# Kernel optimization log

Measured on AMD Instinct MI355X. Metric: run time of the kernel, lower is better.

## Reference

```python
import jax, jax.numpy as jnp
import numpy as np
import math

N_HEADS = 16
ROPE_BASE = 10000.0


def _rope_interleaved(t, cos, sin):
    # t: [B,H,T,dk]; cos/sin: [T, dk//2] broadcast over B,H
    te, to = t[..., 0::2], t[..., 1::2]
    re = te * cos - to * sin
    ro = te * sin + to * cos
    # interleave back: [..., dk//2, 2] -> [..., dk]
    return jnp.stack([re, ro], axis=-1).reshape(t.shape)


def setup_inputs() -> dict:
    key = jax.random.key(0)
    ks = jax.random.split(key, 5)
    B, T, C = 2, 2048, 1024
    s = 1.0 / math.sqrt(C)
    return {
        "x": jax.random.normal(ks[0], (B, T, C), dtype=jnp.float32),
        "W_qkv": jax.random.normal(ks[1], (C, 3 * C), dtype=jnp.float32) * s,
        "b_qkv": jax.random.normal(ks[2], (3 * C,), dtype=jnp.float32) * 0.02,
        "W_proj": jax.random.normal(ks[3], (C, C), dtype=jnp.float32) * s,
        "b_proj": jax.random.normal(ks[4], (C,), dtype=jnp.float32) * 0.02,
    }


def reference(x, W_qkv, b_qkv, W_proj, b_proj):
    B, T, C = x.shape
    H = N_HEADS
    dk = C // H

    qkv = x @ W_qkv + b_qkv                      # [B,T,3C]
    q, k, v = jnp.split(qkv, 3, axis=-1)
    q = q.reshape(B, T, H, dk).transpose(0, 2, 1, 3)  # [B,H,T,dk]
    k = k.reshape(B, T, H, dk).transpose(0, 2, 1, 3)
    v = v.reshape(B, T, H, dk).transpose(0, 2, 1, 3)

    # RoPE angles: pos * base^(-2i/dk)
    freqs = ROPE_BASE ** (-2.0 * jnp.arange(dk // 2, dtype=jnp.float32) / dk)
    angles = jnp.arange(T, dtype=jnp.float32)[:, None] * freqs[None, :]  # [T,dk//2]
    cos, sin = jnp.cos(angles), jnp.sin(angles)

    q = _rope_interleaved(q, cos, sin)
    k = _rope_interleaved(k, cos, sin)

    attn = jnp.einsum("bhqd,bhkd->bhqk", q, k) / math.sqrt(dk)  # [B,H,T,T]
    causal = jnp.triu(jnp.full((T, T), -jnp.inf, dtype=attn.dtype), k=1)
    attn = jax.nn.softmax(attn + causal, axis=-1)

    scores = jnp.einsum("bhqk,bhkd->bhqd", attn, v)  # [B,H,T,dk]
    scores = scores.transpose(0, 2, 1, 3).reshape(B, T, C)
    return scores @ W_proj + b_proj
```

## Files before the change

kernel.cpp:

```cpp
#include <hip/hip_runtime.h>
#include <hip/hip_bf16.h>

typedef __bf16 bf16x8 __attribute__((ext_vector_type(8)));
typedef float f32x4 __attribute__((ext_vector_type(4)));
typedef float f32x16 __attribute__((ext_vector_type(16)));
typedef unsigned short u16;
typedef u16 u16x8 __attribute__((ext_vector_type(8)));

__device__ __forceinline__ u16 f2bf(float f) {
  union { float f; unsigned u; } v; v.f = f;
  unsigned r = v.u + 0x7fffu + ((v.u >> 16) & 1u);
  return (u16)(r >> 16);
}
__device__ __forceinline__ float bf2f(u16 u) {
  union { unsigned u; float f; } v; v.u = (unsigned)u << 16; return v.f;
}
__device__ __forceinline__ unsigned cvtpk(float a, float b) {
  unsigned r;
  asm("v_cvt_pk_bf16_f32 %0, %1, %2" : "=v"(r) : "v"(a), "v"(b));
  return r;
}
__device__ __forceinline__ float exp2_(float x) {
  float r;
  asm("v_exp_f32 %0, %1" : "=v"(r) : "v"(x));
  return r;
}
__device__ __forceinline__ float sin2pi_(float x) {
  float r;
  asm("v_sin_f32 %0, %1" : "=v"(r) : "v"(x));
  return r;
}
__device__ __forceinline__ float cos2pi_(float x) {
  float r;
  asm("v_cos_f32 %0, %1" : "=v"(r) : "v"(x));
  return r;
}
__device__ __forceinline__ void gload16(const void* g, void* l) {
  __builtin_amdgcn_global_load_lds(
      (__attribute__((address_space(1))) void*)(void*)g,
      (__attribute__((address_space(3))) void*)l, 16, 0, 0);
}

union U8 { bf16x8 v; unsigned u[4]; };

__global__ __launch_bounds__(256) void cast_x_k(const float* __restrict__ x,
                                                u16* __restrict__ xb, int n8) {
  int id = blockIdx.x * 256 + threadIdx.x;
  if (id >= n8) return;
  const float4* p = (const float4*)(x + (size_t)id * 8);
  float4 a = p[0], b = p[1];
  u16x8 o;
  o[0] = f2bf(a.x); o[1] = f2bf(a.y); o[2] = f2bf(a.z); o[3] = f2bf(a.w);
  o[4] = f2bf(b.x); o[5] = f2bf(b.y); o[6] = f2bf(b.z); o[7] = f2bf(b.w);
  *(u16x8*)(xb + (size_t)id * 8) = o;
}

__global__ __launch_bounds__(256) void tcast_k(const float* __restrict__ W,
                                               u16* __restrict__ Wt, int R, int Cc) {
  __shared__ float tile[32][33];
  int bx = blockIdx.x * 32, by = blockIdx.y * 32;
  int tx = threadIdx.x & 31, ty = threadIdx.x >> 5;
#pragma unroll
  for (int j = 0; j < 4; j++)
    tile[ty + j * 8][tx] = W[(size_t)(by + ty + j * 8) * Cc + bx + tx];
  __syncthreads();
#pragma unroll
  for (int j = 0; j < 4; j++)
    Wt[(size_t)(bx + ty + j * 8) * R + by + tx] = f2bf(tile[tx][ty + j * 8]);
}

template <bool BF16OUT>
__global__ __launch_bounds__(256) void gemm_bt_k(const u16* __restrict__ A,
                                                 const u16* __restrict__ Bt,
                                                 const float* __restrict__ bias,
                                                 void* __restrict__ Cv,
                                                 int M, int N, int K) {
  __shared__ u16 As[128 * 64];
  __shared__ u16 Bs[128 * 64];
  int tid = threadIdx.x;
  int m0 = blockIdx.y * 128, n0 = blockIdx.x * 128;
  int wave = tid >> 6, lane = tid & 63;
  int wm = (wave & 1) * 64, wn = (wave >> 1) * 64;
  int lrow = lane & 15, lk = (lane >> 4) * 8;
  int rr = lane >> 3, cb = (lane & 7) * 16;

  f32x4 acc[4][4] = {};

  for (int k0 = 0; k0 < K; k0 += 64) {
#pragma unroll
    for (int i = 0; i < 4; i++) {
      int row = wave * 32 + i * 8 + rr;
      int cc = (cb ^ ((row & 7) << 4)) >> 1;
      gload16(A + (size_t)(m0 + row) * K + k0 + cc, &As[(wave * 32 + i * 8) * 64]);
      gload16(Bt + (size_t)(n0 + row) * K + k0 + cc, &Bs[(wave * 32 + i * 8) * 64]);
    }
    __syncthreads();
#pragma unroll
    for (int kk = 0; kk < 2; kk++) {
      bf16x8 af[4], bfr[4];
#pragma unroll
      for (int i = 0; i < 4; i++) {
        int arow = wm + i * 16 + lrow;
        int ab = (arow * 128 + (kk * 32 + lk) * 2) ^ ((arow & 7) << 4);
        af[i] = *(const bf16x8*)((const char*)As + ab);
        int brow = wn + i * 16 + lrow;
        int bb = (brow * 128 + (kk * 32 + lk) * 2) ^ ((brow & 7) << 4);
        bfr[i] = *(const bf16x8*)((const char*)Bs + bb);
      }
#pragma unroll
      for (int i = 0; i < 4; i++)
#pragma unroll
        for (int j = 0; j < 4; j++)
          acc[i][j] = __builtin_amdgcn_mfma_f32_16x16x32_bf16(af[i], bfr[j], acc[i][j], 0, 0, 0);
    }
    __syncthreads();
  }
  int rg = lane >> 4;
#pragma unroll
  for (int i = 0; i < 4; i++) {
#pragma unroll
    for (int j = 0; j < 4; j++) {
      int col = n0 + wn + j * 16 + lrow;
      float bz = bias ? bias[col] : 0.f;
#pragma unroll
      for (int r = 0; r < 4; r++) {
        int row = m0 + wm + i * 16 + rg * 4 + r;
        float val = acc[i][j][r] + bz;
        if constexpr (BF16OUT)
          ((u16*)Cv)[(size_t)row * N + col] = f2bf(val);
        else
          ((float*)Cv)[(size_t)row * N + col] = val;
      }
    }
  }
}

__global__ __launch_bounds__(256) void rope_pack_k(const u16* __restrict__ qkv,
                                                   u16* __restrict__ qf,
                                                   u16* __restrict__ kf,
                                                   u16* __restrict__ vf) {
  __shared__ u16 tl[64][72];
  int bh = blockIdx.x, tb = blockIdx.y;
  int b = bh >> 4, h = bh & 15;
  int tid = threadIdx.x;
  int tloc = tid >> 2;
  int a = tid & 3;
  int tg = tb * 64 + tloc;
  const u16* rowp = qkv + ((size_t)(b * 2048 + tg)) * 3072 + h * 64 + 16 * a;
  u16x8 q0 = *(const u16x8*)(rowp);
  u16x8 q1 = *(const u16x8*)(rowp + 8);
  u16x8 k0 = *(const u16x8*)(rowp + 1024);
  u16x8 k1 = *(const u16x8*)(rowp + 1032);
  const float QS = 0.18033688011112042f;
  const float C1 = -0.41524101186092029f;
  const float C2 = 0.15915494309189535f;
  u16x8 qo0, qo1, ko0, ko1;
#pragma unroll
  for (int j = 0; j < 8; j++) {
    int i = 8 * a + j;
    float fr = (float)tg * (exp2f((float)i * C1) * C2);
    fr = fr - floorf(fr);
    float sv = sin2pi_(fr), cv = cos2pi_(fr);
    float qx, qy, kx, ky;
    if (j < 4) {
      qx = bf2f(q0[2 * j]); qy = bf2f(q0[2 * j + 1]);
      kx = bf2f(k0[2 * j]); ky = bf2f(k0[2 * j + 1]);
    } else {
      qx = bf2f(q1[2 * j - 8]); qy = bf2f(q1[2 * j - 7]);
      kx = bf2f(k1[2 * j - 8]); ky = bf2f(k1[2 * j - 7]);
    }
    u16 qre = f2bf((qx * cv - qy * sv) * QS), qro = f2bf((qx * sv + qy * cv) * QS);
    u16 kre = f2bf(kx * cv - ky * sv),        kro = f2bf(kx * sv + ky * cv);
    if (j < 4) { qo0[2 * j] = qre; qo0[2 * j + 1] = qro; ko0[2 * j] = kre; ko0[2 * j + 1] = kro; }
    else       { qo1[2 * j - 8] = qre; qo1[2 * j - 7] = qro; ko1[2 * j - 8] = kre; ko1[2 * j - 7] = kro; }
  }
  size_t qbase = ((size_t)bh * 64 + (tg >> 5)) * 2048 + a * 512 + (tg & 31) * 8;
  *(u16x8*)(qf + qbase) = qo0;
  *(u16x8*)(qf + qbase + 256) = qo1;
  size_t kbase = (((size_t)bh * 32 + (tg >> 6)) * 2 + ((tg >> 5) & 1)) * 2048 + a * 512 + (tg & 31) * 8;
  *(u16x8*)(kf + kbase) = ko0;
  *(u16x8*)(kf + kbase + 256) = ko1;
#pragma unroll
  for (int rep = 0; rep < 2; rep++) {
    int tr = rep * 32 + (tid >> 3);
    int dc = (tid & 7) * 8;
    u16x8 v = *(const u16x8*)(qkv + ((size_t)(b * 2048 + tb * 64 + tr)) * 3072 + 2048 + h * 64 + dc);
    *(u16x8*)&tl[tr][dc] = v;
  }
  __syncthreads();
  u16* dst = vf + ((size_t)bh * 32 + tb) * 4096;
#pragma unroll
  for (int rep = 0; rep < 2; rep++) {
    int c = rep * 256 + tid;
    int dh = c >> 8, s = (c >> 6) & 3, l = c & 63;
    int hi = l >> 5, ql = l & 31;
    u16x8 o;
#pragma unroll
    for (int j = 0; j < 8; j++) o[j] = tl[s * 16 + hi * 8 + j][dh * 32 + ql];
    *(u16x8*)(dst + (size_t)c * 8) = o;
  }
}


#define KPREF(K0, K1, IT)                                                         \
  do {                                                                            \
    const u16* kb_ = KfP + (size_t)(IT) * 4096 + ln8;                             \
    _Pragma("unroll") for (int d_ = 0; d_ < 4; d_++) {                            \
      K0[d_] = *(const bf16x8*)(kb_ + d_ * 512);                                  \
      K1[d_] = *(const bf16x8*)(kb_ + 2048 + d_ * 512);                           \
    }                                                                             \
  } while (0)

#define QKC(SA, SB, K0, K1)                                                       \
  do {                                                                            \
    SA = (f32x16){};                                                              \
    SB = (f32x16){};                                                              \
    _Pragma("unroll") for (int d_ = 0; d_ < 4; d_++) {                            \
      SA = __builtin_amdgcn_mfma_f32_32x32x16_bf16(K0[d_], qfr[d_], SA, 0, 0, 0); \
      SB = __builtin_amdgcn_mfma_f32_32x32x16_bf16(K1[d_], qfr[d_], SB, 0, 0, 0); \
    }                                                                             \
  } while (0)

#define VLOADM(IT)                                                                \
  do {                                                                            \
    const u16* vb_ = VfP + (size_t)(IT) * 4096 + ln8;                             \
    _Pragma("unroll") for (int s_ = 0; s_ < 4; s_++) {                            \
      vv0[s_] = *(const bf16x8*)(vb_ + s_ * 512);                                 \
      vv1[s_] = *(const bf16x8*)(vb_ + 2048 + s_ * 512);                          \
    }                                                                             \
  } while (0)

#define SMPV(SA, SB, IT, MASKF)                                                   \
  do {                                                                            \
    if (MASKF) {                                                                  \
      int kv0_ = (IT) * 64;                                                       \
      _Pragma("unroll") for (int r_ = 0; r_ < 16; r_++) {                         \
        int ro_ = (r_ & 3) + 8 * (r_ >> 2) + 4 * hi;                              \
        if (kv0_ + ro_ > qg) SA[r_] = -3e38f;                                     \
        if (kv0_ + 32 + ro_ > qg) SB[r_] = -3e38f;                                \
      }                                                                           \
    }                                                                             \
    _Pragma("unroll") for (int r_ = 0; r_ < 16; r_++) {                           \
      SA[r_] = exp2_(SA[r_]);                                                     \
      SB[r_] = exp2_(SB[r_]);                                                     \
    }                                                                             \
    unsigned w0_ = cvtpk(SA[0], SA[1]),   w1_ = cvtpk(SA[2], SA[3]);              \
    unsigned w2_ = cvtpk(SA[4], SA[5]),   w3_ = cvtpk(SA[6], SA[7]);              \
    unsigned w4_ = cvtpk(SA[8], SA[9]),   w5_ = cvtpk(SA[10], SA[11]);            \
    unsigned w6_ = cvtpk(SA[12], SA[13]), w7_ = cvtpk(SA[14], SA[15]);            \
    unsigned y0_ = cvtpk(SB[0], SB[1]),   y1_ = cvtpk(SB[2], SB[3]);              \
    unsigned y2_ = cvtpk(SB[4], SB[5]),   y3_ = cvtpk(SB[6], SB[7]);              \
    unsigned y4_ = cvtpk(SB[8], SB[9]),   y5_ = cvtpk(SB[10], SB[11]);            \
    unsigned y6_ = cvtpk(SB[12], SB[13]), y7_ = cvtpk(SB[14], SB[15]);            \
    asm("v_permlane32_swap_b32 %0, %1" : "+v"(w0_), "+v"(w2_));                   \
    asm("v_permlane32_swap_b32 %0, %1" : "+v"(w1_), "+v"(w3_));                   \
    asm("v_permlane32_swap_b32 %0, %1" : "+v"(w4_), "+v"(w6_));                   \
    asm("v_permlane32_swap_b32 %0, %1" : "+v"(w5_), "+v"(w7_));                   \
    asm("v_permlane32_swap_b32 %0, %1" : "+v"(y0_), "+v"(y2_));                   \
    asm("v_permlane32_swap_b32 %0, %1" : "+v"(y1_), "+v"(y3_));                   \
    asm("v_permlane32_swap_b32 %0, %1" : "+v"(y4_), "+v"(y6_));                   \
    asm("v_permlane32_swap_b32 %0, %1" : "+v"(y5_), "+v"(y7_));                   \
    U8 pf0_, pf1_, pf2_, pf3_;                                                    \
    pf0_.u[0] = w0_; pf0_.u[1] = w1_; pf0_.u[2] = w2_; pf0_.u[3] = w3_;           \
    pf1_.u[0] = w4_; pf1_.u[1] = w5_; pf1_.u[2] = w6_; pf1_.u[3] = w7_;           \
    pf2_.u[0] = y0_; pf2_.u[1] = y1_; pf2_.u[2] = y2_; pf2_.u[3] = y3_;           \
    pf3_.u[0] = y4_; pf3_.u[1] = y5_; pf3_.u[2] = y6_; pf3_.u[3] = y7_;           \
    o0 = __builtin_amdgcn_mfma_f32_32x32x16_bf16(vv0[0], pf0_.v, o0, 0, 0, 0);    \
    o1 = __builtin_amdgcn_mfma_f32_32x32x16_bf16(vv1[0], pf0_.v, o1, 0, 0, 0);    \
    o0 = __builtin_amdgcn_mfma_f32_32x32x16_bf16(vv0[1], pf1_.v, o0, 0, 0, 0);    \
    o1 = __builtin_amdgcn_mfma_f32_32x32x16_bf16(vv1[1], pf1_.v, o1, 0, 0, 0);    \
    o0 = __builtin_amdgcn_mfma_f32_32x32x16_bf16(vv0[2], pf2_.v, o0, 0, 0, 0);    \
    o1 = __builtin_amdgcn_mfma_f32_32x32x16_bf16(vv1[2], pf2_.v, o1, 0, 0, 0);    \
    o0 = __builtin_amdgcn_mfma_f32_32x32x16_bf16(vv0[3], pf3_.v, o0, 0, 0, 0);    \
    o1 = __builtin_amdgcn_mfma_f32_32x32x16_bf16(vv1[3], pf3_.v, o1, 0, 0, 0);    \
    ls = __builtin_amdgcn_mfma_f32_32x32x16_bf16(onesf.v, pf0_.v, ls, 0, 0, 0);   \
    ls = __builtin_amdgcn_mfma_f32_32x32x16_bf16(onesf.v, pf1_.v, ls, 0, 0, 0);   \
    ls = __builtin_amdgcn_mfma_f32_32x32x16_bf16(onesf.v, pf2_.v, ls, 0, 0, 0);   \
    ls = __builtin_amdgcn_mfma_f32_32x32x16_bf16(onesf.v, pf3_.v, ls, 0, 0, 0);   \
  } while (0)

__global__ __launch_bounds__(64) void attn_k(const u16* __restrict__ Qf,
                                             const u16* __restrict__ Kf,
                                             const u16* __restrict__ Vf,
                                             u16* __restrict__ Os) {
  const int T = 2048;
  int blk = blockIdx.x;
  int g = blk & 7;
  int bh = g * 4 + ((blk >> 3) & 3);
  int qt = 63 - (blk >> 5);
  int lane = threadIdx.x & 63;
  int ql = lane & 31, hi = lane >> 5;
  int ln8 = lane * 8;
  int qg = qt * 32 + ql;
  int nIter = (qt >> 1) + 1;
  const u16* QfP = Qf + (size_t)bh * 64 * 2048;
  const u16* KfP = Kf + (size_t)bh * 32 * 4096;
  const u16* VfP = Vf + (size_t)bh * 32 * 4096;
  int b = bh >> 4, h = bh & 15;

  U8 onesf;
#pragma unroll
  for (int j = 0; j < 4; j++) onesf.u[j] = 0x3F803F80u;

  bf16x8 qfr[4];
#pragma unroll
  for (int ds = 0; ds < 4; ds++)
    qfr[ds] = *(const bf16x8*)(QfP + (size_t)qt * 2048 + ds * 512 + ln8);

  f32x16 o0 = {}, o1 = {}, ls = {};
  bf16x8 Ka0[4], Ka1[4], Kb0[4], Kb1[4], vv0[4], vv1[4];
  f32x16 sA0, sA1, sB0, sB1;

  KPREF(Ka0, Ka1, 0);
  QKC(sA0, sA1, Ka0, Ka1);
  if (nIter > 1) KPREF(Kb0, Kb1, 1);

  int t = 0;
  for (;;) {
    bool last = (t == nIter - 1);
    VLOADM(t);
    if (t + 2 < nIter) KPREF(Ka0, Ka1, t + 2);
    if (!last) QKC(sB0, sB1, Kb0, Kb1);
    SMPV(sA0, sA1, t, last);
    if (last) break;
    ++t;
    last = (t == nIter - 1);
    VLOADM(t);
    if (t + 2 < nIter) KPREF(Kb0, Kb1, t + 2);
    if (!last) QKC(sA0, sA1, Ka0, Ka1);
    SMPV(sB0, sB1, t, last);
    if (last) break;
    ++t;
  }

  float inv = 1.f / ls[0];
  u16* orow = Os + ((size_t)(b * T + qg)) * 1024 + h * 64;
#pragma unroll
  for (int j = 0; j < 4; j++) {
    ushort4 o;
    o.x = f2bf(o0[4 * j + 0] * inv); o.y = f2bf(o0[4 * j + 1] * inv);
    o.z = f2bf(o0[4 * j + 2] * inv); o.w = f2bf(o0[4 * j + 3] * inv);
    *(ushort4*)(orow + 8 * j + 4 * hi) = o;
    ushort4 q2;
    q2.x = f2bf(o1[4 * j + 0] * inv); q2.y = f2bf(o1[4 * j + 1] * inv);
    q2.z = f2bf(o1[4 * j + 2] * inv); q2.w = f2bf(o1[4 * j + 3] * inv);
    *(ushort4*)(orow + 32 + 8 * j + 4 * hi) = q2;
  }
}

extern "C" void kernel_launch(void* const* d_in, const int* in_sizes, int n_in,
                              void* d_out, int out_size, void* d_ws, size_t ws_size,
                              hipStream_t stream) {
  const float* x      = (const float*)d_in[0];
  const float* W_qkv  = (const float*)d_in[1];
  const float* b_qkv  = (const float*)d_in[2];
  const float* W_proj = (const float*)d_in[3];
  const float* b_proj = (const float*)d_in[4];
  float* out = (float*)d_out;

  const int B = 2, T = 2048, C = 1024;
  const int M = B * T;

  char* ws = (char*)d_ws;
  u16* xb     = (u16*)(ws);
  u16* wqkvt  = (u16*)(ws + (8ull << 20));
  u16* wprojt = (u16*)(ws + (14ull << 20));
  u16* qfb    = (u16*)(ws + (16ull << 20));
  u16* kfb    = (u16*)(ws + (24ull << 20));
  u16* vfb    = (u16*)(ws + (32ull << 20));
  u16* sc     = (u16*)(ws + (40ull << 20));
  u16* qkvb   = (u16*)(ws + (48ull << 20));

  cast_x_k<<<(M * C / 8 + 255) / 256, 256, 0, stream>>>(x, xb, M * C / 8);
  tcast_k<<<dim3(3 * C / 32, C / 32), 256, 0, stream>>>(W_qkv, wqkvt, C, 3 * C);
  tcast_k<<<dim3(C / 32, C / 32), 256, 0, stream>>>(W_proj, wprojt, C, C);
  gemm_bt_k<true><<<dim3(3 * C / 128, M / 128), 256, 0, stream>>>(xb, wqkvt, b_qkv, qkvb, M, 3 * C, C);
  rope_pack_k<<<dim3(B * 16, T / 64), 256, 0, stream>>>(qkvb, qfb, kfb, vfb);
  attn_k<<<2048, 64, 0, stream>>>(qfb, kfb, vfb, sc);
  gemm_bt_k<false><<<dim3(C / 128, M / 128), 256, 0, stream>>>(sc, wprojt, b_proj, out, M, C, C);
}
```

Baseline: 119.1 us.

## Split causal attention KV range across blocks and merge partials

Long causal query tiles are split along the key range: tiles 32-63 into 4 slots and tiles 16-31 into 2, so attn_k launches 5632 smaller blocks instead of 2048 unevenly sized ones. Each slot writes an unnormalized bf16 partial output and its row sum, and a new mrg_k kernel adds the partials and normalizes. The goal is to remove the load imbalance and tail effect of causal attention. In exchange it adds an extra kernel launch, extra global traffic for the partial buffers, and rounding of unnormalized partials to bf16. The workspace layout is rearranged so the partial buffers reuse regions whose data has already been consumed.

After: 130.0 us. 9.2% more time.

```diff
diff --git a/kernel.cpp b/kernel.cpp
--- a/kernel.cpp
+++ b/kernel.cpp
@@ -282,17 +282,24 @@
 __global__ __launch_bounds__(64) void attn_k(const u16* __restrict__ Qf,
                                              const u16* __restrict__ Kf,
                                              const u16* __restrict__ Vf,
-                                             u16* __restrict__ Os) {
+                                             u16* __restrict__ pO,
+                                             float* __restrict__ pL) {
   const int T = 2048;
   int blk = blockIdx.x;
-  int g = blk & 7;
-  int bh = g * 4 + ((blk >> 3) & 3);
-  int qt = 63 - (blk >> 5);
+  int bh = (blk & 7) * 4 + ((blk >> 3) & 3);
+  int c = blk >> 5;
+  int qt, slot;
+  if (c < 128)      { qt = 32 + (c >> 2);        slot = c & 3; }
+  else if (c < 160) { qt = 16 + ((c - 128) >> 1); slot = (c - 128) & 1; }
+  else              { qt = c - 160;               slot = 0; }
+  int nTot = (qt >> 1) + 1;
+  int nslots = (qt < 16) ? 1 : (qt < 32 ? 2 : 4);
+  int it0 = (nTot * slot) / nslots;
+  int itEnd = (nTot * (slot + 1)) / nslots;
   int lane = threadIdx.x & 63;
   int ql = lane & 31, hi = lane >> 5;
   int ln8 = lane * 8;
   int qg = qt * 32 + ql;
-  int nIter = (qt >> 1) + 1;
   const u16* QfP = Qf + (size_t)bh * 64 * 2048;
   const u16* KfP = Kf + (size_t)bh * 32 * 4096;
   const u16* VfP = Vf + (size_t)bh * 32 * 4096;
@@ -311,41 +318,67 @@
   bf16x8 Ka0[4], Ka1[4], Kb0[4], Kb1[4], vv0[4], vv1[4];
   f32x16 sA0, sA1, sB0, sB1;
 
-  KPREF(Ka0, Ka1, 0);
+  int t = it0;
+  KPREF(Ka0, Ka1, t);
   QKC(sA0, sA1, Ka0, Ka1);
-  if (nIter > 1) KPREF(Kb0, Kb1, 1);
-
-  int t = 0;
+  if (t + 1 < itEnd) KPREF(Kb0, Kb1, t + 1);
+
   for (;;) {
-    bool last = (t == nIter - 1);
+    bool last = (t == itEnd - 1);
     VLOADM(t);
-    if (t + 2 < nIter) KPREF(Ka0, Ka1, t + 2);
+    if (t + 2 < itEnd) KPREF(Ka0, Ka1, t + 2);
     if (!last) QKC(sB0, sB1, Kb0, Kb1);
-    SMPV(sA0, sA1, t, last);
+    SMPV(sA0, sA1, t, t == nTot - 1);
     if (last) break;
     ++t;
-    last = (t == nIter - 1);
+    last = (t == itEnd - 1);
     VLOADM(t);
-    if (t + 2 < nIter) KPREF(Kb0, Kb1, t + 2);
+    if (t + 2 < itEnd) KPREF(Kb0, Kb1, t + 2);
     if (!last) QKC(sA0, sA1, Ka0, Ka1);
-    SMPV(sB0, sB1, t, last);
+    SMPV(sB0, sB1, t, t == nTot - 1);
     if (last) break;
     ++t;
   }
 
-  float inv = 1.f / ls[0];
-  u16* orow = Os + ((size_t)(b * T + qg)) * 1024 + h * 64;
+  u16* orow = pO + (size_t)slot * 4194304 + ((size_t)(b * T + qg)) * 1024 + h * 64;
 #pragma unroll
   for (int j = 0; j < 4; j++) {
     ushort4 o;
-    o.x = f2bf(o0[4 * j + 0] * inv); o.y = f2bf(o0[4 * j + 1] * inv);
-    o.z = f2bf(o0[4 * j + 2] * inv); o.w = f2bf(o0[4 * j + 3] * inv);
+    o.x = f2bf(o0[4 * j + 0]); o.y = f2bf(o0[4 * j + 1]);
+    o.z = f2bf(o0[4 * j + 2]); o.w = f2bf(o0[4 * j + 3]);
     *(ushort4*)(orow + 8 * j + 4 * hi) = o;
     ushort4 q2;
-    q2.x = f2bf(o1[4 * j + 0] * inv); q2.y = f2bf(o1[4 * j + 1] * inv);
-    q2.z = f2bf(o1[4 * j + 2] * inv); q2.w = f2bf(o1[4 * j + 3] * inv);
+    q2.x = f2bf(o1[4 * j + 0]); q2.y = f2bf(o1[4 * j + 1]);
+    q2.z = f2bf(o1[4 * j + 2]); q2.w = f2bf(o1[4 * j + 3]);
     *(ushort4*)(orow + 32 + 8 * j + 4 * hi) = q2;
   }
+  if (hi == 0) pL[slot * 65536 + bh * 2048 + qg] = ls[0];
+}
+
+__global__ __launch_bounds__(256) void mrg_k(const u16* __restrict__ pO,
+                                             const float* __restrict__ pL,
+                                             u16* __restrict__ sc) {
+  int id = blockIdx.x * 256 + threadIdx.x;
+  int col8 = id & 127;
+  int row = id >> 7;
+  int t = row & 2047, b = row >> 11;
+  int h = col8 >> 3;
+  int qt = t >> 5;
+  int ns = (qt < 16) ? 1 : (qt < 32 ? 2 : 4);
+  int bh = b * 16 + h;
+  float acc[8] = {};
+  float lsum = 0.f;
+  for (int s = 0; s < ns; s++) {
+    lsum += pL[s * 65536 + bh * 2048 + t];
+    u16x8 v = *(const u16x8*)(pO + (size_t)s * 4194304 + (size_t)id * 8);
+#pragma unroll
+    for (int j = 0; j < 8; j++) acc[j] += bf2f(v[j]);
+  }
+  float inv = 1.f / lsum;
+  u16x8 o;
+#pragma unroll
+  for (int j = 0; j < 8; j++) o[j] = f2bf(acc[j] * inv);
+  *(u16x8*)(sc + (size_t)id * 8) = o;
 }
 
 extern "C" void kernel_launch(void* const* d_in, const int* in_sizes, int n_in,
@@ -362,20 +395,23 @@
   const int M = B * T;
 
   char* ws = (char*)d_ws;
-  u16* xb     = (u16*)(ws);
-  u16* wqkvt  = (u16*)(ws + (8ull << 20));
-  u16* wprojt = (u16*)(ws + (14ull << 20));
-  u16* qfb    = (u16*)(ws + (16ull << 20));
-  u16* kfb    = (u16*)(ws + (24ull << 20));
-  u16* vfb    = (u16*)(ws + (32ull << 20));
-  u16* sc     = (u16*)(ws + (40ull << 20));
-  u16* qkvb   = (u16*)(ws + (48ull << 20));
+  u16* wprojt = (u16*)(ws);
+  u16* xb     = (u16*)(ws + (2ull << 20));
+  u16* wqkvt  = (u16*)(ws + (10ull << 20));
+  u16* qkvb   = (u16*)(ws + (16ull << 20));
+  u16* pO     = (u16*)(ws + (2ull << 20));
+  float* pL   = (float*)(ws + (34ull << 20));
+  u16* qfb    = (u16*)(ws + (40ull << 20));
+  u16* kfb    = (u16*)(ws + (48ull << 20));
+  u16* vfb    = (u16*)(ws + (56ull << 20));
+  u16* sc     = (u16*)(ws + (64ull << 20));
 
   cast_x_k<<<(M * C / 8 + 255) / 256, 256, 0, stream>>>(x, xb, M * C / 8);
   tcast_k<<<dim3(3 * C / 32, C / 32), 256, 0, stream>>>(W_qkv, wqkvt, C, 3 * C);
   tcast_k<<<dim3(C / 32, C / 32), 256, 0, stream>>>(W_proj, wprojt, C, C);
   gemm_bt_k<true><<<dim3(3 * C / 128, M / 128), 256, 0, stream>>>(xb, wqkvt, b_qkv, qkvb, M, 3 * C, C);
   rope_pack_k<<<dim3(B * 16, T / 64), 256, 0, stream>>>(qkvb, qfb, kfb, vfb);
-  attn_k<<<2048, 64, 0, stream>>>(qfb, kfb, vfb, sc);
+  attn_k<<<5632, 64, 0, stream>>>(qfb, kfb, vfb, pO, pL);
+  mrg_k<<<M * C / 8 / 256, 256, 0, stream>>>(pO, pL, sc);
   gemm_bt_k<false><<<dim3(C / 128, M / 128), 256, 0, stream>>>(sc, wprojt, b_proj, out, M, C, C);
 }
```
